# Performance work log

Measured on AMD Instinct MI355X. Metric: run time of the kernel, lower is better.

## Reference

```python
import jax, jax.numpy as jnp
import numpy as np

B, N, NP, NS = 8, 4096, 1024, 32
CF = 64            # input point-feature channels; in_channel = 3 + CF = 67
MLP = [64, 128, 256]
EPS = 1e-5         # BatchNorm eps (torch default)


def setup_inputs() -> dict:
    key = jax.random.key(0)
    ks = jax.random.split(key, 8)
    inp = {
        "xyz": jax.random.normal(ks[0], (B, N, 3), jnp.float32),
        "points": jax.random.normal(ks[1], (B, CF, N), jnp.float32),
        "sample_idx": jax.random.randint(ks[2], (B, NP), 0, N, dtype=jnp.int32),
        "neighbor_idx": jax.random.randint(ks[3], (B, NP, NS), 0, N, dtype=jnp.int32),
    }
    c = 3 + CF
    for i, o in enumerate(MLP):
        wk = jax.random.fold_in(ks[4], i)
        inp[f"W{i}"] = jax.random.normal(wk, (o, c), jnp.float32) * (1.0 / np.sqrt(c))
        inp[f"b{i}"] = jnp.zeros((o,), jnp.float32)
        inp[f"gamma{i}"] = jnp.ones((o,), jnp.float32)
        inp[f"beta{i}"] = jnp.zeros((o,), jnp.float32)
        c = o
    return inp


def _forward(xyz, points, sample_idx, neighbor_idx, params):
    # xyz: (B,N,3)  points: (B,CF,N)
    new_xyz = jnp.take_along_axis(xyz, sample_idx[:, :, None], axis=1)        # (B,NP,3)
    nbr_xyz = jax.vmap(lambda x, idx: x[idx])(xyz, neighbor_idx)               # (B,NP,NS,3)
    rel = nbr_xyz - new_xyz[:, :, None, :]                                     # (B,NP,NS,3)
    nbr_feat = jax.vmap(lambda f, idx: f[:, idx])(points, neighbor_idx)        # (B,CF,NP,NS)
    x = jnp.concatenate([rel.transpose(0, 3, 1, 2), nbr_feat], axis=1)         # (B,3+CF,NP,NS)
    # 1x1 Conv2d -> BatchNorm2d (training-mode batch stats) -> ReLU stack
    for W, b, g, be in params:
        x = jnp.einsum('oc,bcps->bops', W, x) + b[None, :, None, None]
        mu = x.mean(axis=(0, 2, 3), keepdims=True)
        var = x.var(axis=(0, 2, 3), keepdims=True)
        x = g[None, :, None, None] * (x - mu) * jax.lax.rsqrt(var + EPS) + be[None, :, None, None]
        x = jax.nn.relu(x)
    new_points = x.max(axis=-1)                                                # (B,C_out,NP)
    return new_xyz, new_points


def reference(xyz, points, sample_idx, neighbor_idx,
              W0, b0, gamma0, beta0,
              W1, b1, gamma1, beta1,
              W2, b2, gamma2, beta2):
    params = [(W0, b0, gamma0, beta0), (W1, b1, gamma1, beta1), (W2, b2, gamma2, beta2)]
    return _forward(xyz, points, sample_idx, neighbor_idx, params)
```

## Files before the change

kernel.cpp:

```cpp
#include <hip/hip_runtime.h>

typedef unsigned short u16;
typedef unsigned int u32;
typedef __attribute__((ext_vector_type(8))) short short8;
typedef __attribute__((ext_vector_type(16))) float f32x16;

#define BB 8
#define NN 4096
#define NPP 1024
#define NSS 32
#define CFF 64
#define C0 67
#define H0 64
#define H1 128
#define H2 256
#define MTOT (BB*NPP*NSS)
#define BN_EPS 1e-5f
#define INV_M (1.0f/262144.0f)

#define MFMA32(a,b,c) __builtin_amdgcn_mfma_f32_32x32x16_bf16(a,b,c,0,0,0)

__device__ __forceinline__ float bf2f(u16 h){ return __uint_as_float(((u32)h)<<16); }
__device__ __forceinline__ u16 f2bf(float f){
  u32 u = __float_as_uint(f);
  u32 r = (u + 0x7fffu + ((u>>16)&1u)) >> 16;
  return (u16)r;
}
__device__ __forceinline__ u32 pack2(float a, float b){
  return (u32)f2bf(a) | ((u32)f2bf(b)<<16);
}

#define WS_NEED 46280704u

__global__ __launch_bounds__(256) void k_setup(
    const float* __restrict__ xyz, const float* __restrict__ points,
    const int* __restrict__ sidx,
    const float* __restrict__ W0, const float* __restrict__ W1, const float* __restrict__ W2,
    u16* __restrict__ ptsT, u16* __restrict__ Wt0c, u16* __restrict__ Wt1c,
    u16* __restrict__ Wt2c, float* __restrict__ out_newxyz)
{
  int blk = blockIdx.x, tid = threadIdx.x;
  if (blk < 512) {
    __shared__ float t[64][65];
    int b = blk >> 6, n0 = (blk & 63) << 6;
    int nloc = tid & 63, cpart = tid >> 6;
    for (int i = 0; i < 16; ++i) {
      int c = i*4 + cpart;
      t[c][nloc] = points[(size_t)(b*CFF + c)*NN + n0 + nloc];
    }
    __syncthreads();
    int cloc = tid & 63, npart = tid >> 6;
    for (int i = 0; i < 16; ++i) {
      int n = i*4 + npart;
      ptsT[((size_t)(b*NN + n0 + n))*CFF + cloc] = f2bf(t[cloc][n]);
    }
  } else if (blk < 544) {
    int t0 = (blk - 512)*256 + tid;
    int b = t0 >> 10;
    int s = sidx[t0];
    for (int k = 0; k < 3; ++k)
      out_newxyz[(size_t)t0*3 + k] = xyz[((size_t)(b*NN + s))*3 + k];
  } else if (blk == 544) {
    for (int i = 0; i < 24; ++i) {
      int e = i*256 + tid;
      int kc = e >> 9, o = (e >> 3) & 63, j = e & 7, k = kc*8 + j;
      float v = (k < 64) ? W0[o*C0 + 3 + k] : ((k < 67) ? W0[o*C0 + (k - 64)] : 0.f);
      Wt0c[e] = f2bf(v);
    }
  } else if (blk == 545) {
    for (int i = 0; i < 32; ++i) {
      int e = i*256 + tid;
      int kc = e >> 10, n = (e >> 3) & 127, j = e & 7;
      Wt1c[e] = f2bf(W1[n*H0 + kc*8 + j]);
    }
  } else {
    int base = (blk - 546) * 4096;
    for (int i = 0; i < 16; ++i) {
      int e = base + i*256 + tid;
      int kc = e >> 11, n = (e >> 3) & 255, j = e & 7;
      Wt2c[e] = f2bf(W2[n*H1 + kc*8 + j]);
    }
  }
}

__global__ __launch_bounds__(256) void k_xyz_only(
    const float* __restrict__ xyz, const int* __restrict__ sidx, float* __restrict__ out_newxyz)
{
  int t0 = blockIdx.x*256 + threadIdx.x;
  int b = t0 >> 10;
  int s = sidx[t0];
  for (int k = 0; k < 3; ++k)
    out_newxyz[(size_t)t0*3 + k] = xyz[((size_t)(b*NN + s))*3 + k];
}

__global__ __launch_bounds__(256) void k_l0(
    const float* __restrict__ xyz, const int* __restrict__ sidx, const int* __restrict__ nidx,
    const u16* __restrict__ ptsT, const u16* __restrict__ Wt0c,
    u16* __restrict__ y0, float* __restrict__ stats)
{
  __shared__ u16 XLc[12*128*8];
  __shared__ u16 W0c[12*64*8];
  int tid = threadIdx.x;
  int m0 = blockIdx.x * 128;
  int b = m0 >> 15;

  for (int i = 0; i < 3; ++i)
    ((uint4*)W0c)[i*256 + tid] = ((const uint4*)Wt0c)[i*256 + tid];

  int pos = tid & 127, half = tid >> 7;
  int m = m0 + pos;
  int nb = nidx[m];
  {
    const uint4* prow = (const uint4*)(ptsT + ((size_t)(b*NN + nb))*CFF + half*32);
    uint4 h0 = prow[0], h1 = prow[1], h2 = prow[2], h3 = prow[3];
    *(uint4*)&XLc[((half*4+0)*128 + pos)*8] = h0;
    *(uint4*)&XLc[((half*4+1)*128 + pos)*8] = h1;
    *(uint4*)&XLc[((half*4+2)*128 + pos)*8] = h2;
    *(uint4*)&XLc[((half*4+3)*128 + pos)*8] = h3;
    if (half == 0) {
      int p = (m & 32767) >> 5;
      int sp = sidx[b*NPP + p];
      float r0 = xyz[((size_t)(b*NN+nb))*3+0] - xyz[((size_t)(b*NN+sp))*3+0];
      float r1 = xyz[((size_t)(b*NN+nb))*3+1] - xyz[((size_t)(b*NN+sp))*3+1];
      float r2 = xyz[((size_t)(b*NN+nb))*3+2] - xyz[((size_t)(b*NN+sp))*3+2];
      uint4 v = { pack2(r0, r1), pack2(r2, 0.f), 0u, 0u };
      *(uint4*)&XLc[(8*128 + pos)*8] = v;
    } else {
      uint4 z = {0u,0u,0u,0u};
      *(uint4*)&XLc[(9*128 + pos)*8]  = z;
      *(uint4*)&XLc[(10*128 + pos)*8] = z;
      *(uint4*)&XLc[(11*128 + pos)*8] = z;
    }
  }
  __syncthreads();

  int lane = tid & 63, wv = tid >> 6;
  int l31 = lane & 31, kh = lane >> 5;
  int nt = wv & 1, mtb = (wv >> 1) * 2;
  f32x16 acc[2];
  for (int mi = 0; mi < 2; ++mi) for (int r = 0; r < 16; ++r) acc[mi][r] = 0.f;

  for (int kt = 0; kt < 6; ++kt) {
    int ck = kt*2 + kh;
    short8 bfrag = *(const short8*)&W0c[(ck*64 + nt*32 + l31)*8];
    for (int mi = 0; mi < 2; ++mi) {
      short8 afrag = *(const short8*)&XLc[(ck*128 + (mtb+mi)*32 + l31)*8];
      acc[mi] = MFMA32(afrag, bfrag, acc[mi]);
    }
  }

  float s = 0.f, q = 0.f;
  for (int mi = 0; mi < 2; ++mi)
    for (int r = 0; r < 16; ++r) { float y = acc[mi][r]; s += y; q += y*y; }
  s += __shfl_xor(s, 32); q += __shfl_xor(q, 32);
  if (lane < 32) {
    int slot = blockIdx.x & 7;
    atomicAdd(&stats[slot*256 + nt*32 + lane], s);
    atomicAdd(&stats[2048 + slot*256 + nt*32 + lane], q);
  }
  for (int mi = 0; mi < 2; ++mi)
    for (int r = 0; r < 16; ++r) {
      int mm = (mtb+mi)*32 + (r&3) + 8*(r>>2) + 4*kh;
      y0[(size_t)(m0+mm)*H0 + nt*32 + l31] = f2bf(acc[mi][r]);
    }
}

__global__ __launch_bounds__(256) void k_l1s(
    const u16* __restrict__ y0, const u16* __restrict__ Wt1c,
    const float* __restrict__ g0, const float* __restrict__ e0,
    const float* __restrict__ stIn, float* __restrict__ stOut)
{
  __shared__ u16 X0c[8*128*8];
  __shared__ u16 W1c[8*128*8];
  __shared__ float scl0[64], sft0[64];
  int tid = threadIdx.x;
  int m0 = blockIdx.x * 128;

  if (tid < 64) {
    float s = 0.f, q = 0.f;
    for (int sl = 0; sl < 8; ++sl) { s += stIn[sl*256 + tid]; q += stIn[2048 + sl*256 + tid]; }
    float mu = s*INV_M, var = q*INV_M - mu*mu;
    float sc = g0[tid] * rsqrtf(var + BN_EPS);
    scl0[tid] = sc; sft0[tid] = e0[tid] - mu*sc;
  }
  for (int i = 0; i < 4; ++i)
    ((uint4*)W1c)[i*256 + tid] = ((const uint4*)Wt1c)[i*256 + tid];

  int pos = tid & 127, half = tid >> 7;
  {
    const u16* row = y0 + (size_t)(m0 + pos)*H0 + half*32;
    u16 hs[32];
    for (int t = 0; t < 4; ++t) *(uint4*)&hs[t*8] = ((const uint4*)row)[t];
    __syncthreads();
    u16 ob[32];
    for (int j = 0; j < 32; ++j) {
      int c = half*32 + j;
      ob[j] = f2bf(fmaxf(fmaf(scl0[c], bf2f(hs[j]), sft0[c]), 0.f));
    }
    for (int t = 0; t < 4; ++t)
      *(uint4*)&X0c[((half*4+t)*128 + pos)*8] = *(uint4*)&ob[t*8];
  }
  __syncthreads();

  int lane = tid & 63, wv = tid >> 6;
  int l31 = lane & 31, kh = lane >> 5;
  f32x16 acc[4];
  for (int mt = 0; mt < 4; ++mt) for (int r = 0; r < 16; ++r) acc[mt][r] = 0.f;

  for (int kt = 0; kt < 4; ++kt) {
    int ck = kt*2 + kh;
    short8 bfrag = *(const short8*)&W1c[(ck*128 + wv*32 + l31)*8];
    for (int mt = 0; mt < 4; ++mt) {
      short8 afrag = *(const short8*)&X0c[(ck*128 + mt*32 + l31)*8];
      acc[mt] = MFMA32(afrag, bfrag, acc[mt]);
    }
  }

  float s = 0.f, q = 0.f;
  for (int mt = 0; mt < 4; ++mt)
    for (int r = 0; r < 16; ++r) { float y = acc[mt][r]; s += y; q += y*y; }
  s += __shfl_xor(s, 32); q += __shfl_xor(q, 32);
  if (lane < 32) {
    int slot = blockIdx.x & 7;
    atomicAdd(&stOut[slot*256 + wv*32 + lane], s);
    atomicAdd(&stOut[2048 + slot*256 + wv*32 + lane], q);
  }
}

__global__ __launch_bounds__(256) void k_l2f(
    const u16* __restrict__ y0, const u16* __restrict__ Wt1c, const u16* __restrict__ Wt2c,
    const float* __restrict__ g0, const float* __restrict__ e0,
    const float* __restrict__ g1, const float* __restrict__ e1,
    const float* __restrict__ st0, const float* __restrict__ st1, float* __restrict__ stOut,
    u16* __restrict__ mxp, u16* __restrict__ mnp)
{
  __shared__ u16 X1c[16*64*8];
  __shared__ u16 UB[16384];
  __shared__ float scl0[64], sft0[64], scl1[128], sft1[128];
  int tid = threadIdx.x;
  int m0 = blockIdx.x * 64;

  if (tid < 64) {
    float s = 0.f, q = 0.f;
    for (int sl = 0; sl < 8; ++sl) { s += st0[sl*256 + tid]; q += st0[2048 + sl*256 + tid]; }
    float mu = s*INV_M, var = q*INV_M - mu*mu;
    float sc = g0[tid] * rsqrtf(var + BN_EPS);
    scl0[tid] = sc; sft0[tid] = e0[tid] - mu*sc;
  }
  if (tid < 128) {
    float s = 0.f, q = 0.f;
    for (int sl = 0; sl < 8; ++sl) { s += st1[sl*256 + tid]; q += st1[2048 + sl*256 + tid]; }
    float mu = s*INV_M, var = q*INV_M - mu*mu;
    float sc = g1[tid] * rsqrtf(var + BN_EPS);
    scl1[tid] = sc; sft1[tid] = e1[tid] - mu*sc;
  }
  u16* X0c = UB;
  u16* W1c = UB + 4096;
  for (int i = 0; i < 4; ++i)
    ((uint4*)W1c)[i*256 + tid] = ((const uint4*)Wt1c)[i*256 + tid];

  int pos = tid & 63, grp = tid >> 6;
  {
    const u16* row = y0 + (size_t)(m0 + pos)*H0 + grp*16;
    u16 hs[16];
    *(uint4*)&hs[0] = ((const uint4*)row)[0];
    *(uint4*)&hs[8] = ((const uint4*)row)[1];
    __syncthreads();
    u16 ob[16];
    for (int j = 0; j < 16; ++j) {
      int c = grp*16 + j;
      ob[j] = f2bf(fmaxf(fmaf(scl0[c], bf2f(hs[j]), sft0[c]), 0.f));
    }
    *(uint4*)&X0c[((2*grp)*64 + pos)*8]   = *(uint4*)&ob[0];
    *(uint4*)&X0c[((2*grp+1)*64 + pos)*8] = *(uint4*)&ob[8];
  }
  __syncthreads();

  int lane = tid & 63, wv = tid >> 6;
  int l31 = lane & 31, kh = lane >> 5;

  f32x16 acc1[2];
  for (int mt = 0; mt < 2; ++mt) for (int r = 0; r < 16; ++r) acc1[mt][r] = 0.f;
  for (int kt = 0; kt < 4; ++kt) {
    int ck = kt*2 + kh;
    short8 bfrag = *(const short8*)&W1c[(ck*128 + wv*32 + l31)*8];
    for (int mt = 0; mt < 2; ++mt) {
      short8 afrag = *(const short8*)&X0c[(ck*64 + mt*32 + l31)*8];
      acc1[mt] = MFMA32(afrag, bfrag, acc1[mt]);
    }
  }

  {
    int ch = wv*32 + l31;
    int cb = ch >> 3, cr = ch & 7;
    float sc1 = scl1[ch], sf1 = sft1[ch];
    for (int mt = 0; mt < 2; ++mt)
      for (int r = 0; r < 16; ++r) {
        int mm = mt*32 + (r&3) + 8*(r>>2) + 4*kh;
        X1c[(cb*64 + mm)*8 + cr] = f2bf(fmaxf(fmaf(sc1, acc1[mt][r], sf1), 0.f));
      }
  }
  __syncthreads();

  f32x16 acc2[2][2];
  for (int nt = 0; nt < 2; ++nt) for (int mt = 0; mt < 2; ++mt)
    for (int r = 0; r < 16; ++r) acc2[nt][mt][r] = 0.f;

  for (int h = 0; h < 2; ++h) {
    for (int i = 0; i < 8; ++i)
      ((uint4*)UB)[i*256 + tid] = ((const uint4*)Wt2c)[h*2048 + i*256 + tid];
    __syncthreads();
    for (int k4 = 0; k4 < 4; ++k4) {
      int ckx = (h*4 + k4)*2 + kh;
      int ckw = k4*2 + kh;
      short8 a[2], bf_[2];
      for (int mt = 0; mt < 2; ++mt) a[mt]  = *(const short8*)&X1c[(ckx*64 + mt*32 + l31)*8];
      for (int nt = 0; nt < 2; ++nt) bf_[nt] = *(const short8*)&UB[(ckw*256 + wv*64 + nt*32 + l31)*8];
      for (int nt = 0; nt < 2; ++nt)
        for (int mt = 0; mt < 2; ++mt)
          acc2[nt][mt] = MFMA32(a[mt], bf_[nt], acc2[nt][mt]);
    }
    __syncthreads();
  }

  int slot = blockIdx.x & 7;
  for (int nt = 0; nt < 2; ++nt) {
    float s = 0.f, q = 0.f;
    float mx[2] = {-3.0e38f, -3.0e38f}, mn[2] = {3.0e38f, 3.0e38f};
    for (int mt = 0; mt < 2; ++mt)
      for (int r = 0; r < 16; ++r) {
        float y = acc2[nt][mt][r];
        s += y; q += y*y;
        mx[mt] = fmaxf(mx[mt], y); mn[mt] = fminf(mn[mt], y);
      }
    s += __shfl_xor(s, 32); q += __shfl_xor(q, 32);
    mx[0] = fmaxf(mx[0], __shfl_xor(mx[0], 32));
    mx[1] = fmaxf(mx[1], __shfl_xor(mx[1], 32));
    mn[0] = fminf(mn[0], __shfl_xor(mn[0], 32));
    mn[1] = fminf(mn[1], __shfl_xor(mn[1], 32));
    if (lane < 32) {
      int c = wv*64 + nt*32 + lane;
      atomicAdd(&stOut[slot*256 + c], s);
      atomicAdd(&stOut[2048 + slot*256 + c], q);
      for (int mt = 0; mt < 2; ++mt) {
        size_t pr = (size_t)blockIdx.x*2 + mt;
        mxp[pr*H2 + c] = f2bf(mx[mt]);
        mnp[pr*H2 + c] = f2bf(mn[mt]);
      }
    }
  }
}

__global__ __launch_bounds__(256) void k_final(
    const u16* __restrict__ mxp, const u16* __restrict__ mnp,
    const float* __restrict__ gma, const float* __restrict__ bta,
    const float* __restrict__ stIn, float* __restrict__ out_np)
{
  __shared__ float tmp[256][33];
  int tid = threadIdx.x;
  int b = blockIdx.x >> 5;
  int p0 = (blockIdx.x & 31) * 32;

  float s = 0.f, q = 0.f;
  for (int sl = 0; sl < 8; ++sl) { s += stIn[sl*256 + tid]; q += stIn[2048 + sl*256 + tid]; }
  float mu = s*INV_M, var = q*INV_M - mu*mu;
  float sc = gma[tid] * rsqrtf(var + BN_EPS);
  float sh = bta[tid] - mu*sc;

  for (int pp = 0; pp < 32; ++pp) {
    size_t base = ((size_t)(b*NPP + p0 + pp))*H2 + tid;
    float xv = bf2f(mxp[base]), nv = bf2f(mnp[base]);
    float v = (sc >= 0.f) ? fmaf(sc, xv, sh) : fmaf(sc, nv, sh);
    tmp[tid][pp] = fmaxf(v, 0.f);
  }
  __syncthreads();

  int pl = tid & 31, cg = tid >> 5;
  for (int cc = 0; cc < 32; ++cc) {
    int c = cc*8 + cg;
    out_np[((size_t)b*H2 + c)*NPP + p0 + pl] = tmp[c][pl];
  }
}

extern "C" void kernel_launch(void* const* d_in, const int* in_sizes, int n_in,
                              void* d_out, int out_size, void* d_ws, size_t ws_size,
                              hipStream_t stream)
{
  const float* xyz    = (const float*)d_in[0];
  const float* points = (const float*)d_in[1];
  const int*   sidx   = (const int*)d_in[2];
  const int*   nidx   = (const int*)d_in[3];
  const float* W0 = (const float*)d_in[4];
  const float* g0 = (const float*)d_in[6];
  const float* e0 = (const float*)d_in[7];
  const float* W1 = (const float*)d_in[8];
  const float* g1 = (const float*)d_in[10];
  const float* e1 = (const float*)d_in[11];
  const float* W2 = (const float*)d_in[12];
  const float* g2 = (const float*)d_in[14];
  const float* e2 = (const float*)d_in[15];

  float* out_xyz = (float*)d_out;
  float* out_np  = out_xyz + (size_t)BB*NPP*3;

  if (ws_size < (size_t)WS_NEED) {
    hipMemsetAsync(out_np, 0, (size_t)BB*H2*NPP*4, stream);
    k_xyz_only<<<32, 256, 0, stream>>>(xyz, sidx, out_xyz);
    return;
  }

  char* ws = (char*)d_ws;
  float* stats = (float*)(ws + 0);
  u16*   Wt0c  = (u16*)(ws + 49152);
  u16*   Wt1c  = (u16*)(ws + 61440);
  u16*   Wt2c  = (u16*)(ws + 77824);
  u16*   ptsT  = (u16*)(ws + 143360);
  u16*   y0    = (u16*)(ws + 4337664);
  u16*   mxp   = (u16*)(ws + 37892096);
  u16*   mnp   = (u16*)(ws + 42086400);

  hipMemsetAsync(stats, 0, 3*4096*sizeof(float), stream);
  k_setup<<<554, 256, 0, stream>>>(xyz, points, sidx, W0, W1, W2,
                                   ptsT, Wt0c, Wt1c, Wt2c, out_xyz);
  k_l0<<<MTOT/128, 256, 0, stream>>>(xyz, sidx, nidx, ptsT, Wt0c, y0, stats);
  k_l1s<<<MTOT/128, 256, 0, stream>>>(y0, Wt1c, g0, e0, stats, stats + 4096);
  k_l2f<<<MTOT/64, 256, 0, stream>>>(y0, Wt1c, Wt2c, g0, e0, g1, e1,
                                     stats, stats + 4096, stats + 8192, mxp, mnp);
  k_final<<<256, 256, 0, stream>>>(mxp, mnp, g2, e2, stats + 8192, out_np);
}
```

Measured before the change: 178.6 us.

## Precompute layer-0 conv per input point and gather instead of per-neighbor GEMM

Layer 0 is linear, so W0·[xyz_nb - xyz_center; f_nb] is split into U[nb] - T[center]. U and T are computed once per input point (32K points instead of 262K neighbor rows), and later kernels gather them. This removes the per-neighbor layer-0 GEMM, the transposed points buffer and the large y0 intermediate. A lightweight stats kernel gathers U-T to compute BN0 statistics. The layer-1 output is also repacked into a padded LDS layout with vectorized writes. The cost is extra gathers of both U and T rows in each consumer kernel, plus double bf16 rounding before the subtraction.

```diff
diff --git a/kernel.cpp b/kernel.cpp
--- a/kernel.cpp
+++ b/kernel.cpp
@@ -14,6 +14,7 @@
 #define H0 64
 #define H1 128
 #define H2 256
+#define NTOT (BB*NN)
 #define MTOT (BB*NPP*NSS)
 #define BN_EPS 1e-5f
 #define INV_M (1.0f/262144.0f)
@@ -30,51 +31,40 @@
   return (u32)f2bf(a) | ((u32)f2bf(b)<<16);
 }
 
-#define WS_NEED 46280704u
+#define WS_NEED 16918528u
 
 __global__ __launch_bounds__(256) void k_setup(
-    const float* __restrict__ xyz, const float* __restrict__ points,
-    const int* __restrict__ sidx,
+    const float* __restrict__ xyz, const int* __restrict__ sidx,
     const float* __restrict__ W0, const float* __restrict__ W1, const float* __restrict__ W2,
-    u16* __restrict__ ptsT, u16* __restrict__ Wt0c, u16* __restrict__ Wt1c,
-    u16* __restrict__ Wt2c, float* __restrict__ out_newxyz)
+    u16* __restrict__ Wt0c, u16* __restrict__ Wt1c, u16* __restrict__ Wt2c,
+    float* __restrict__ out_newxyz)
 {
   int blk = blockIdx.x, tid = threadIdx.x;
-  if (blk < 512) {
-    __shared__ float t[64][65];
-    int b = blk >> 6, n0 = (blk & 63) << 6;
-    int nloc = tid & 63, cpart = tid >> 6;
-    for (int i = 0; i < 16; ++i) {
-      int c = i*4 + cpart;
-      t[c][nloc] = points[(size_t)(b*CFF + c)*NN + n0 + nloc];
-    }
-    __syncthreads();
-    int cloc = tid & 63, npart = tid >> 6;
-    for (int i = 0; i < 16; ++i) {
-      int n = i*4 + npart;
-      ptsT[((size_t)(b*NN + n0 + n))*CFF + cloc] = f2bf(t[cloc][n]);
-    }
-  } else if (blk < 544) {
-    int t0 = (blk - 512)*256 + tid;
+  if (blk < 32) {
+    int t0 = blk*256 + tid;
     int b = t0 >> 10;
     int s = sidx[t0];
     for (int k = 0; k < 3; ++k)
       out_newxyz[(size_t)t0*3 + k] = xyz[((size_t)(b*NN + s))*3 + k];
-  } else if (blk == 544) {
-    for (int i = 0; i < 24; ++i) {
+  } else if (blk == 32) {
+    for (int i = 0; i < 20; ++i) {
       int e = i*256 + tid;
-      int kc = e >> 9, o = (e >> 3) & 63, j = e & 7, k = kc*8 + j;
-      float v = (k < 64) ? W0[o*C0 + 3 + k] : ((k < 67) ? W0[o*C0 + (k - 64)] : 0.f);
+      if (e >= 5120) break;
+      int kc = e >> 9, o = (e >> 3) & 63, j = e & 7;
+      float v;
+      if (kc < 8)       v = W0[o*C0 + 3 + kc*8 + j];
+      else if (kc == 8) v = (j < 3) ? W0[o*C0 + j] : 0.f;
+      else              v = 0.f;
       Wt0c[e] = f2bf(v);
     }
-  } else if (blk == 545) {
+  } else if (blk == 33) {
     for (int i = 0; i < 32; ++i) {
       int e = i*256 + tid;
       int kc = e >> 10, n = (e >> 3) & 127, j = e & 7;
       Wt1c[e] = f2bf(W1[n*H0 + kc*8 + j]);
     }
   } else {
-    int base = (blk - 546) * 4096;
+    int base = (blk - 34) * 4096;
     for (int i = 0; i < 16; ++i) {
       int e = base + i*256 + tid;
       int kc = e >> 11, n = (e >> 3) & 255, j = e & 7;
@@ -93,80 +83,124 @@
     out_newxyz[(size_t)t0*3 + k] = xyz[((size_t)(b*NN + s))*3 + k];
 }
 
-__global__ __launch_bounds__(256) void k_l0(
-    const float* __restrict__ xyz, const int* __restrict__ sidx, const int* __restrict__ nidx,
-    const u16* __restrict__ ptsT, const u16* __restrict__ Wt0c,
-    u16* __restrict__ y0, float* __restrict__ stats)
-{
-  __shared__ u16 XLc[12*128*8];
-  __shared__ u16 W0c[12*64*8];
+__global__ __launch_bounds__(256) void k_uv(
+    const float* __restrict__ xyz, const float* __restrict__ points,
+    const u16* __restrict__ Wt0c, u16* __restrict__ U, u16* __restrict__ T)
+{
+  __shared__ u16 XLc[10*128*8];
+  __shared__ u16 W0c[10*64*8];
   int tid = threadIdx.x;
-  int m0 = blockIdx.x * 128;
-  int b = m0 >> 15;
-
-  for (int i = 0; i < 3; ++i)
-    ((uint4*)W0c)[i*256 + tid] = ((const uint4*)Wt0c)[i*256 + tid];
-
-  int pos = tid & 127, half = tid >> 7;
-  int m = m0 + pos;
-  int nb = nidx[m];
+  int gn0 = blockIdx.x * 128;
+  int b = gn0 >> 12;
+  int n0 = gn0 & 4095;
+
+  for (int i = 0; i < 3; ++i) {
+    int e = i*256 + tid;
+    if (e < 640) ((uint4*)W0c)[e] = ((const uint4*)Wt0c)[e];
+  }
   {
-    const uint4* prow = (const uint4*)(ptsT + ((size_t)(b*NN + nb))*CFF + half*32);
-    uint4 h0 = prow[0], h1 = prow[1], h2 = prow[2], h3 = prow[3];
-    *(uint4*)&XLc[((half*4+0)*128 + pos)*8] = h0;
-    *(uint4*)&XLc[((half*4+1)*128 + pos)*8] = h1;
-    *(uint4*)&XLc[((half*4+2)*128 + pos)*8] = h2;
-    *(uint4*)&XLc[((half*4+3)*128 + pos)*8] = h3;
-    if (half == 0) {
-      int p = (m & 32767) >> 5;
-      int sp = sidx[b*NPP + p];
-      float r0 = xyz[((size_t)(b*NN+nb))*3+0] - xyz[((size_t)(b*NN+sp))*3+0];
-      float r1 = xyz[((size_t)(b*NN+nb))*3+1] - xyz[((size_t)(b*NN+sp))*3+1];
-      float r2 = xyz[((size_t)(b*NN+nb))*3+2] - xyz[((size_t)(b*NN+sp))*3+2];
-      uint4 v = { pack2(r0, r1), pack2(r2, 0.f), 0u, 0u };
-      *(uint4*)&XLc[(8*128 + pos)*8] = v;
-    } else {
-      uint4 z = {0u,0u,0u,0u};
-      *(uint4*)&XLc[(9*128 + pos)*8]  = z;
-      *(uint4*)&XLc[(10*128 + pos)*8] = z;
-      *(uint4*)&XLc[(11*128 + pos)*8] = z;
-    }
-  }
-  __syncthreads();
-
-  int lane = tid & 63, wv = tid >> 6;
-  int l31 = lane & 31, kh = lane >> 5;
-  int nt = wv & 1, mtb = (wv >> 1) * 2;
-  f32x16 acc[2];
-  for (int mi = 0; mi < 2; ++mi) for (int r = 0; r < 16; ++r) acc[mi][r] = 0.f;
-
-  for (int kt = 0; kt < 6; ++kt) {
+    int c = tid >> 2, nseg = tid & 3;
+    const float* src = points + ((size_t)(b*CFF + c))*NN + n0 + nseg*32;
+    int cb = c >> 3, cr = c & 7;
+    for (int t = 0; t < 8; ++t) {
+      float4 v = *(const float4*)(src + t*4);
+      int n = nseg*32 + t*4;
+      XLc[(cb*128 + n+0)*8 + cr] = f2bf(v.x);
+      XLc[(cb*128 + n+1)*8 + cr] = f2bf(v.y);
+      XLc[(cb*128 + n+2)*8 + cr] = f2bf(v.z);
+      XLc[(cb*128 + n+3)*8 + cr] = f2bf(v.w);
+    }
+  }
+  if (tid < 128) {
+    int gn = gn0 + tid;
+    float x = xyz[(size_t)gn*3+0], y = xyz[(size_t)gn*3+1], z = xyz[(size_t)gn*3+2];
+    uint4 v = { pack2(x,y), pack2(z,0.f), 0u, 0u };
+    *(uint4*)&XLc[(8*128 + tid)*8] = v;
+  } else {
+    uint4 z4 = {0u,0u,0u,0u};
+    *(uint4*)&XLc[(9*128 + (tid-128))*8] = z4;
+  }
+  __syncthreads();
+
+  int lane = tid & 63, wv = tid >> 6, l31 = lane & 31, kh = lane >> 5;
+  int nt = wv & 1, mtb = (wv >> 1)*2;
+  f32x16 accT2[2], accU2[2];
+  for (int mi = 0; mi < 2; ++mi) for (int r = 0; r < 16; ++r) accT2[mi][r] = 0.f;
+
+  {
+    int ck = 8 + kh;
+    short8 bfrag = *(const short8*)&W0c[(ck*64 + nt*32 + l31)*8];
+    for (int mi = 0; mi < 2; ++mi) {
+      short8 afrag = *(const short8*)&XLc[(ck*128 + (mtb+mi)*32 + l31)*8];
+      accT2[mi] = MFMA32(afrag, bfrag, accT2[mi]);
+    }
+  }
+  for (int mi = 0; mi < 2; ++mi) accU2[mi] = accT2[mi];
+  for (int kt = 0; kt < 4; ++kt) {
     int ck = kt*2 + kh;
     short8 bfrag = *(const short8*)&W0c[(ck*64 + nt*32 + l31)*8];
     for (int mi = 0; mi < 2; ++mi) {
       short8 afrag = *(const short8*)&XLc[(ck*128 + (mtb+mi)*32 + l31)*8];
-      acc[mi] = MFMA32(afrag, bfrag, acc[mi]);
-    }
-  }
-
-  float s = 0.f, q = 0.f;
-  for (int mi = 0; mi < 2; ++mi)
-    for (int r = 0; r < 16; ++r) { float y = acc[mi][r]; s += y; q += y*y; }
-  s += __shfl_xor(s, 32); q += __shfl_xor(q, 32);
-  if (lane < 32) {
-    int slot = blockIdx.x & 7;
-    atomicAdd(&stats[slot*256 + nt*32 + lane], s);
-    atomicAdd(&stats[2048 + slot*256 + nt*32 + lane], q);
-  }
+      accU2[mi] = MFMA32(afrag, bfrag, accU2[mi]);
+    }
+  }
+
+  int c = nt*32 + l31;
   for (int mi = 0; mi < 2; ++mi)
     for (int r = 0; r < 16; ++r) {
-      int mm = (mtb+mi)*32 + (r&3) + 8*(r>>2) + 4*kh;
-      y0[(size_t)(m0+mm)*H0 + nt*32 + l31] = f2bf(acc[mi][r]);
-    }
+      int gm = gn0 + (mtb+mi)*32 + (r&3) + 8*(r>>2) + 4*kh;
+      U[(size_t)gm*64 + c] = f2bf(accU2[mi][r]);
+      T[(size_t)gm*64 + c] = f2bf(accT2[mi][r]);
+    }
+}
+
+__global__ __launch_bounds__(256) void k_s0(
+    const int* __restrict__ sidx, const int* __restrict__ nidx,
+    const u16* __restrict__ U, const u16* __restrict__ T, float* __restrict__ stats)
+{
+  int tid = threadIdx.x;
+  int m0 = blockIdx.x * 128;
+  int b = m0 >> 15;
+  int c0 = (tid & 15) * 4;
+  int rg = tid >> 4;
+  int mbase = m0 + rg*8;
+  int p = (mbase & 32767) >> 5;
+  int sp = sidx[b*NPP + p];
+  u16 tv[4];
+  *(uint2*)tv = *(const uint2*)(T + ((size_t)(b*NN + sp))*64 + c0);
+  float t0 = bf2f(tv[0]), t1 = bf2f(tv[1]), t2 = bf2f(tv[2]), t3 = bf2f(tv[3]);
+  float s0=0.f,s1=0.f,s2=0.f,s3=0.f,q0=0.f,q1=0.f,q2=0.f,q3=0.f;
+  for (int i = 0; i < 8; ++i) {
+    int nb = nidx[mbase + i];
+    u16 uv[4];
+    *(uint2*)uv = *(const uint2*)(U + ((size_t)(b*NN + nb))*64 + c0);
+    float d0 = bf2f(uv[0]) - t0; s0 += d0; q0 += d0*d0;
+    float d1 = bf2f(uv[1]) - t1; s1 += d1; q1 += d1*d1;
+    float d2 = bf2f(uv[2]) - t2; s2 += d2; q2 += d2*d2;
+    float d3 = bf2f(uv[3]) - t3; s3 += d3; q3 += d3*d3;
+  }
+  for (int msk = 16; msk <= 32; msk <<= 1) {
+    s0 += __shfl_xor(s0, msk); s1 += __shfl_xor(s1, msk);
+    s2 += __shfl_xor(s2, msk); s3 += __shfl_xor(s3, msk);
+    q0 += __shfl_xor(q0, msk); q1 += __shfl_xor(q1, msk);
+    q2 += __shfl_xor(q2, msk); q3 += __shfl_xor(q3, msk);
+  }
+  if ((tid & 63) < 16) {
+    int slot = (blockIdx.x*4 + (tid >> 6)) & 7;
+    atomicAdd(&stats[slot*256 + c0+0], s0);
+    atomicAdd(&stats[slot*256 + c0+1], s1);
+    atomicAdd(&stats[slot*256 + c0+2], s2);
+    atomicAdd(&stats[slot*256 + c0+3], s3);
+    atomicAdd(&stats[2048 + slot*256 + c0+0], q0);
+    atomicAdd(&stats[2048 + slot*256 + c0+1], q1);
+    atomicAdd(&stats[2048 + slot*256 + c0+2], q2);
+    atomicAdd(&stats[2048 + slot*256 + c0+3], q3);
+  }
 }
 
 __global__ __launch_bounds__(256) void k_l1s(
-    const u16* __restrict__ y0, const u16* __restrict__ Wt1c,
+    const int* __restrict__ sidx, const int* __restrict__ nidx,
+    const u16* __restrict__ U, const u16* __restrict__ T, const u16* __restrict__ Wt1c,
     const float* __restrict__ g0, const float* __restrict__ e0,
     const float* __restrict__ stIn, float* __restrict__ stOut)
 {
@@ -175,6 +209,7 @@
   __shared__ float scl0[64], sft0[64];
   int tid = threadIdx.x;
   int m0 = blockIdx.x * 128;
+  int b = m0 >> 15;
 
   if (tid < 64) {
     float s = 0.f, q = 0.f;
@@ -188,22 +223,30 @@
 
   int pos = tid & 127, half = tid >> 7;
   {
-    const u16* row = y0 + (size_t)(m0 + pos)*H0 + half*32;
-    u16 hs[32];
-    for (int t = 0; t < 4; ++t) *(uint4*)&hs[t*8] = ((const uint4*)row)[t];
+    int m = m0 + pos;
+    int nb = nidx[m];
+    int p = (m & 32767) >> 5;
+    int sp = sidx[b*NPP + p];
+    const u16* urow = U + ((size_t)(b*NN + nb))*64 + half*32;
+    const u16* trow = T + ((size_t)(b*NN + sp))*64 + half*32;
+    u16 us[32], ts[32];
+    for (int t = 0; t < 4; ++t) {
+      *(uint4*)&us[t*8] = ((const uint4*)urow)[t];
+      *(uint4*)&ts[t*8] = ((const uint4*)trow)[t];
+    }
     __syncthreads();
     u16 ob[32];
     for (int j = 0; j < 32; ++j) {
       int c = half*32 + j;
-      ob[j] = f2bf(fmaxf(fmaf(scl0[c], bf2f(hs[j]), sft0[c]), 0.f));
+      float d = bf2f(us[j]) - bf2f(ts[j]);
+      ob[j] = f2bf(fmaxf(fmaf(scl0[c], d, sft0[c]), 0.f));
     }
     for (int t = 0; t < 4; ++t)
       *(uint4*)&X0c[((half*4+t)*128 + pos)*8] = *(uint4*)&ob[t*8];
   }
   __syncthreads();
 
-  int lane = tid & 63, wv = tid >> 6;
-  int l31 = lane & 31, kh = lane >> 5;
+  int lane = tid & 63, wv = tid >> 6, l31 = lane & 31, kh = lane >> 5;
   f32x16 acc[4];
   for (int mt = 0; mt < 4; ++mt) for (int r = 0; r < 16; ++r) acc[mt][r] = 0.f;
 
@@ -228,17 +271,20 @@
 }
 
 __global__ __launch_bounds__(256) void k_l2f(
-    const u16* __restrict__ y0, const u16* __restrict__ Wt1c, const u16* __restrict__ Wt2c,
+    const int* __restrict__ sidx, const int* __restrict__ nidx,
+    const u16* __restrict__ U, const u16* __restrict__ T,
+    const u16* __restrict__ Wt1c, const u16* __restrict__ Wt2c,
     const float* __restrict__ g0, const float* __restrict__ e0,
     const float* __restrict__ g1, const float* __restrict__ e1,
     const float* __restrict__ st0, const float* __restrict__ st1, float* __restrict__ stOut,
     u16* __restrict__ mxp, u16* __restrict__ mnp)
 {
-  __shared__ u16 X1c[16*64*8];
+  __shared__ u16 X1c[16*520];
   __shared__ u16 UB[16384];
   __shared__ float scl0[64], sft0[64], scl1[128], sft1[128];
   int tid = threadIdx.x;
   int m0 = blockIdx.x * 64;
+  int b = m0 >> 15;
 
   if (tid < 64) {
     float s = 0.f, q = 0.f;
@@ -261,44 +307,60 @@
 
   int pos = tid & 63, grp = tid >> 6;
   {
-    const u16* row = y0 + (size_t)(m0 + pos)*H0 + grp*16;
-    u16 hs[16];
-    *(uint4*)&hs[0] = ((const uint4*)row)[0];
-    *(uint4*)&hs[8] = ((const uint4*)row)[1];
+    int m = m0 + pos;
+    int nb = nidx[m];
+    int p = (m & 32767) >> 5;
+    int sp = sidx[b*NPP + p];
+    const u16* urow = U + ((size_t)(b*NN + nb))*64 + grp*16;
+    const u16* trow = T + ((size_t)(b*NN + sp))*64 + grp*16;
+    u16 us[16], ts[16];
+    *(uint4*)&us[0] = ((const uint4*)urow)[0];
+    *(uint4*)&us[8] = ((const uint4*)urow)[1];
+    *(uint4*)&ts[0] = ((const uint4*)trow)[0];
+    *(uint4*)&ts[8] = ((const uint4*)trow)[1];
     __syncthreads();
     u16 ob[16];
     for (int j = 0; j < 16; ++j) {
       int c = grp*16 + j;
-      ob[j] = f2bf(fmaxf(fmaf(scl0[c], bf2f(hs[j]), sft0[c]), 0.f));
+      float d = bf2f(us[j]) - bf2f(ts[j]);
+      ob[j] = f2bf(fmaxf(fmaf(scl0[c], d, sft0[c]), 0.f));
     }
     *(uint4*)&X0c[((2*grp)*64 + pos)*8]   = *(uint4*)&ob[0];
     *(uint4*)&X0c[((2*grp+1)*64 + pos)*8] = *(uint4*)&ob[8];
   }
   __syncthreads();
 
-  int lane = tid & 63, wv = tid >> 6;
-  int l31 = lane & 31, kh = lane >> 5;
+  int lane = tid & 63, wv = tid >> 6, l31 = lane & 31, kh = lane >> 5;
 
   f32x16 acc1[2];
-  for (int mt = 0; mt < 2; ++mt) for (int r = 0; r < 16; ++r) acc1[mt][r] = 0.f;
+  for (int nt = 0; nt < 2; ++nt) for (int r = 0; r < 16; ++r) acc1[nt][r] = 0.f;
   for (int kt = 0; kt < 4; ++kt) {
     int ck = kt*2 + kh;
-    short8 bfrag = *(const short8*)&W1c[(ck*128 + wv*32 + l31)*8];
-    for (int mt = 0; mt < 2; ++mt) {
-      short8 afrag = *(const short8*)&X0c[(ck*64 + mt*32 + l31)*8];
-      acc1[mt] = MFMA32(afrag, bfrag, acc1[mt]);
-    }
-  }
+    short8 afrag = *(const short8*)&W1c[(ck*128 + wv*32 + l31)*8];
+    for (int nt = 0; nt < 2; ++nt) {
+      short8 bfrag = *(const short8*)&X0c[(ck*64 + nt*32 + l31)*8];
+      acc1[nt] = MFMA32(afrag, bfrag, acc1[nt]);
+    }
+  }
+  __syncthreads();
 
   {
-    int ch = wv*32 + l31;
-    int cb = ch >> 3, cr = ch & 7;
-    float sc1 = scl1[ch], sf1 = sft1[ch];
-    for (int mt = 0; mt < 2; ++mt)
-      for (int r = 0; r < 16; ++r) {
-        int mm = mt*32 + (r&3) + 8*(r>>2) + 4*kh;
-        X1c[(cb*64 + mm)*8 + cr] = f2bf(fmaxf(fmaf(sc1, acc1[mt][r], sf1), 0.f));
+    float s1r[16], f1r[16];
+    for (int r = 0; r < 16; ++r) {
+      int ch = wv*32 + (r&3) + 8*(r>>2) + 4*kh;
+      s1r[r] = scl1[ch]; f1r[r] = sft1[ch];
+    }
+    for (int nt = 0; nt < 2; ++nt) {
+      int posn = nt*32 + l31;
+      for (int g = 0; g < 4; ++g) {
+        float v0 = fmaxf(fmaf(s1r[g*4+0], acc1[nt][g*4+0], f1r[g*4+0]), 0.f);
+        float v1 = fmaxf(fmaf(s1r[g*4+1], acc1[nt][g*4+1], f1r[g*4+1]), 0.f);
+        float v2 = fmaxf(fmaf(s1r[g*4+2], acc1[nt][g*4+2], f1r[g*4+2]), 0.f);
+        float v3 = fmaxf(fmaf(s1r[g*4+3], acc1[nt][g*4+3], f1r[g*4+3]), 0.f);
+        uint2 w = { pack2(v0, v1), pack2(v2, v3) };
+        *(uint2*)&X1c[(wv*4 + g)*520 + posn*8 + 4*kh] = w;
       }
+    }
   }
   __syncthreads();
 
@@ -314,7 +376,7 @@
       int ckx = (h*4 + k4)*2 + kh;
       int ckw = k4*2 + kh;
       short8 a[2], bf_[2];
-      for (int mt = 0; mt < 2; ++mt) a[mt]  = *(const short8*)&X1c[(ckx*64 + mt*32 + l31)*8];
+      for (int mt = 0; mt < 2; ++mt) a[mt]  = *(const short8*)&X1c[ckx*520 + (mt*32 + l31)*8];
       for (int nt = 0; nt < 2; ++nt) bf_[nt] = *(const short8*)&UB[(ckw*256 + wv*64 + nt*32 + l31)*8];
       for (int nt = 0; nt < 2; ++nt)
         for (int mt = 0; mt < 2; ++mt)
@@ -412,19 +474,21 @@
   char* ws = (char*)d_ws;
   float* stats = (float*)(ws + 0);
   u16*   Wt0c  = (u16*)(ws + 49152);
-  u16*   Wt1c  = (u16*)(ws + 61440);
-  u16*   Wt2c  = (u16*)(ws + 77824);
-  u16*   ptsT  = (u16*)(ws + 143360);
-  u16*   y0    = (u16*)(ws + 4337664);
-  u16*   mxp   = (u16*)(ws + 37892096);
-  u16*   mnp   = (u16*)(ws + 42086400);
+  u16*   Wt1c  = (u16*)(ws + 59392);
+  u16*   Wt2c  = (u16*)(ws + 75776);
+  u16*   Ubuf  = (u16*)(ws + 141312);
+  u16*   Tbuf  = (u16*)(ws + 4335616);
+  u16*   mxp   = (u16*)(ws + 8529920);
+  u16*   mnp   = (u16*)(ws + 12724224);
 
   hipMemsetAsync(stats, 0, 3*4096*sizeof(float), stream);
-  k_setup<<<554, 256, 0, stream>>>(xyz, points, sidx, W0, W1, W2,
-                                   ptsT, Wt0c, Wt1c, Wt2c, out_xyz);
-  k_l0<<<MTOT/128, 256, 0, stream>>>(xyz, sidx, nidx, ptsT, Wt0c, y0, stats);
-  k_l1s<<<MTOT/128, 256, 0, stream>>>(y0, Wt1c, g0, e0, stats, stats + 4096);
-  k_l2f<<<MTOT/64, 256, 0, stream>>>(y0, Wt1c, Wt2c, g0, e0, g1, e1,
+  k_setup<<<42, 256, 0, stream>>>(xyz, sidx, W0, W1, W2, Wt0c, Wt1c, Wt2c, out_xyz);
+  k_uv<<<NTOT/128, 256, 0, stream>>>(xyz, points, Wt0c, Ubuf, Tbuf);
+  k_s0<<<MTOT/128, 256, 0, stream>>>(sidx, nidx, Ubuf, Tbuf, stats);
+  k_l1s<<<MTOT/128, 256, 0, stream>>>(sidx, nidx, Ubuf, Tbuf, Wt1c, g0, e0,
+                                      stats, stats + 4096);
+  k_l2f<<<MTOT/64, 256, 0, stream>>>(sidx, nidx, Ubuf, Tbuf, Wt1c, Wt2c,
+                                     g0, e0, g1, e1,
                                      stats, stats + 4096, stats + 8192, mxp, mnp);
   k_final<<<256, 256, 0, stream>>>(mxp, mnp, g2, e2, stats + 8192, out_np);
 }
```

Result: slower. 264.8 us (+48.3%).
